# Kernel optimization log

Measured on AMD Instinct MI355X. Metric: run time of the kernel, lower is better.

Reference implementation:

```python
import jax, jax.numpy as jnp
import numpy as np

N_NODES = 100000
N_EDGES = 3200000
IN_F, HID, N_CLS = 10, 64, 10
NEG_SLOPE = 0.01  # torch default for F.leaky_relu


def gcn_conv(h, src, dst, W, b, n_nodes):
    h = h @ W  # transform first (small feature dim -> cheap)
    # self loops
    loop = jnp.arange(n_nodes, dtype=src.dtype)
    s = jnp.concatenate([src, loop])
    d = jnp.concatenate([dst, loop])
    deg = jax.ops.segment_sum(jnp.ones_like(d, dtype=h.dtype), d, num_segments=n_nodes)
    dinv = jnp.where(deg > 0, jax.lax.rsqrt(deg), 0.0)
    norm = dinv[s] * dinv[d]  # [E+N]
    msg = h[s] * norm[:, None]  # gather + scale
    out = jax.ops.segment_sum(msg, d, num_segments=n_nodes)  # scatter-add
    return out + b


def setup_inputs() -> dict:
    key = jax.random.key(0)
    ks = jax.random.split(key, 10)
    x = jax.random.normal(ks[0], (N_NODES, IN_F), dtype=jnp.float32)
    edge_index = jax.random.randint(ks[1], (2, N_EDGES), 0, N_NODES, dtype=jnp.int64)
    def glorot(k, fan_in, fan_out):
        lim = np.sqrt(6.0 / (fan_in + fan_out))
        return jax.random.uniform(k, (fan_in, fan_out), jnp.float32, -lim, lim)
    W1 = glorot(ks[2], IN_F, HID)
    b1 = jnp.zeros((HID,), jnp.float32)
    W2 = glorot(ks[3], HID, HID)
    b2 = jnp.zeros((HID,), jnp.float32)
    W3 = glorot(ks[4], HID, HID)
    b3 = jnp.zeros((HID,), jnp.float32)
    Wfc = glorot(ks[5], HID, N_CLS)
    bfc = jnp.zeros((N_CLS,), jnp.float32)
    return {"x": x, "edge_index": edge_index, "W1": W1, "b1": b1,
            "W2": W2, "b2": b2, "W3": W3, "b3": b3, "Wfc": Wfc, "bfc": bfc}


def reference(x, edge_index, W1, b1, W2, b2, W3, b3, Wfc, bfc):
    src, dst = edge_index[0], edge_index[1]
    n = x.shape[0]
    h = jax.nn.leaky_relu(gcn_conv(x, src, dst, W1, b1, n), NEG_SLOPE)
    h = jax.nn.leaky_relu(gcn_conv(h, src, dst, W2, b2, n), NEG_SLOPE)
    h = jax.nn.leaky_relu(gcn_conv(h, src, dst, W3, b3, n), NEG_SLOPE)
    return h @ Wfc + bfc
```

## Files before the change

### kernel.cpp

```cpp
#include <hip/hip_runtime.h>
#include <hip/hip_fp16.h>

#define N_NODES_C 100000
#define N_EDGES_C 3200000
#define IN_F_C 10
#define HID_C 64
#define N_CLS_C 10
#define NEG_SLOPE_C 0.01f

#define NBUCK 98
#define BCAP  36864
#define TILE  2048

typedef _Float16 f16x2 __attribute__((ext_vector_type(2)));

__device__ __forceinline__ float fdot2(unsigned int a, unsigned int b, float c) {
#if defined(__has_builtin) && __has_builtin(__builtin_amdgcn_fdot2)
    return __builtin_amdgcn_fdot2(__builtin_bit_cast(f16x2, a), __builtin_bit_cast(f16x2, b), c, false);
#else
    __half2 ah = __builtin_bit_cast(__half2, a), bh = __builtin_bit_cast(__half2, b);
    float2 af = __half22float2(ah), bf = __half22float2(bh);
    return c + af.x * bf.x + af.y * bf.y;
#endif
}

__global__ __launch_bounds__(256) void k_bucket(const int* __restrict__ src,
                                                const int* __restrict__ dst,
                                                int* __restrict__ bcur,
                                                int* __restrict__ pairs, int E) {
    __shared__ int lcnt[NBUCK];
    __shared__ int gbase[NBUCK];
    const int t = threadIdx.x;
    for (int i = t; i < NBUCK; i += 256) lcnt[i] = 0;
    __syncthreads();
    const int base = blockIdx.x * TILE;
    int p[8], r[8], nb[8];
#pragma unroll
    for (int i = 0; i < 8; ++i) {
        int e = base + t + i * 256;
        if (e < E) {
            int s = src[e], d = dst[e];
            int b = d >> 10;
            nb[i] = b;
            p[i] = (s << 10) | (d & 1023);
            r[i] = atomicAdd(&lcnt[b], 1);
        }
    }
    __syncthreads();
    for (int i = t; i < NBUCK; i += 256)
        gbase[i] = lcnt[i] ? atomicAdd(&bcur[i], lcnt[i]) : 0;
    __syncthreads();
#pragma unroll
    for (int i = 0; i < 8; ++i) {
        int e = base + t + i * 256;
        if (e < E) {
            int pos = gbase[nb[i]] + r[i];
            if (pos < BCAP) pairs[nb[i] * BCAP + pos] = p[i];
        }
    }
}

__global__ __launch_bounds__(128) void k_bscan(const int* __restrict__ bcur,
                                               int* __restrict__ bOff, int nbk) {
    __shared__ int s[128];
    int t = threadIdx.x;
    int v = (t < nbk) ? bcur[t] : 0;
    s[t] = v;
    __syncthreads();
    for (int off = 1; off < 128; off <<= 1) {
        int u = (t >= off) ? s[t - off] : 0;
        __syncthreads();
        s[t] += u;
        __syncthreads();
    }
    if (t < nbk) bOff[t] = s[t] - v;
}

__global__ __launch_bounds__(1024) void k_build(const int* __restrict__ pairs,
                                                const int* __restrict__ bcur,
                                                const int* __restrict__ bOff,
                                                int* __restrict__ row_ptr,
                                                float* __restrict__ dinv,
                                                int* __restrict__ col) {
    __shared__ int hist[1024];
    __shared__ int sm[1024];
    const int b = blockIdx.x;
    const int t = threadIdx.x;
    const int n = min(bcur[b], BCAP);
    const int base = bOff[b];
    const int* pp = pairs + b * BCAP;

    hist[t] = 0;
    __syncthreads();
    for (int i = t; i < n; i += 1024) atomicAdd(&hist[pp[i] & 1023], 1);
    __syncthreads();
    int c = hist[t];
    sm[t] = c;
    __syncthreads();
    for (int off = 1; off < 1024; off <<= 1) {
        int u = (t >= off) ? sm[t - off] : 0;
        __syncthreads();
        sm[t] += u;
        __syncthreads();
    }
    int rp = base + sm[t] - c;
    int gnode = (b << 10) + t;
    if (gnode < N_NODES_C) {
        row_ptr[gnode] = rp;
        dinv[gnode] = rsqrtf((float)(c + 1));
        if (gnode == N_NODES_C - 1) row_ptr[N_NODES_C] = rp + c;
    }
    __syncthreads();
    sm[t] = rp;
    __syncthreads();
    for (int i = t; i < n; i += 1024) {
        int p = pp[i];
        int idx = atomicAdd(&sm[p & 1023], 1);
        col[idx] = p >> 10;
    }
}

__global__ __launch_bounds__(256) void k_mm0(const float* __restrict__ x,
                                             const float* __restrict__ W,
                                             const float* __restrict__ dinv,
                                             __half* __restrict__ hs, int n) {
    __shared__ float4 W4[IN_F_C * 16];
    const int t = threadIdx.x;
    for (int i = t; i < IN_F_C * 16; i += 256) {
        int k = i >> 4, f4 = i & 15;
        W4[i] = ((const float4*)(W + k * HID_C))[f4];
    }
    __syncthreads();
    int idx = blockIdx.x * 256 + t;
    if (idx >= n * 16) return;
    int nn = idx >> 4, f4 = idx & 15;
    const float* row = x + nn * IN_F_C;
    float4 acc = make_float4(0.f, 0.f, 0.f, 0.f);
#pragma unroll
    for (int k = 0; k < IN_F_C; ++k) {
        float xv = row[k];
        float4 w = W4[k * 16 + f4];
        acc.x += xv * w.x; acc.y += xv * w.y; acc.z += xv * w.z; acc.w += xv * w.w;
    }
    float di = dinv[nn];
    ((__half2*)hs)[(nn << 5) + 2 * f4]     = __floats2half2_rn(acc.x * di, acc.y * di);
    ((__half2*)hs)[(nn << 5) + 2 * f4 + 1] = __floats2half2_rn(acc.z * di, acc.w * di);
}

__global__ __launch_bounds__(256) void k_wcvt(const float* __restrict__ W, uint4* __restrict__ wh) {
    int i = blockIdx.x * 256 + threadIdx.x;
    if (i >= 8 * HID_C) return;
    int k8 = i >> 6, f = i & 63;
    __half2 h[4];
#pragma unroll
    for (int j = 0; j < 4; ++j)
        h[j] = __floats2half2_rn(W[(8 * k8 + 2 * j) * HID_C + f],
                                 W[(8 * k8 + 2 * j + 1) * HID_C + f]);
    wh[i] = *(uint4*)h;
}

__global__ __launch_bounds__(256) void k_gftL(const int* __restrict__ row_ptr,
                                              const int* __restrict__ col,
                                              const __half2* __restrict__ hs,
                                              const float* __restrict__ dinv,
                                              const float* __restrict__ bias,
                                              const uint4* __restrict__ wh,
                                              __half* __restrict__ hnext, int n) {
    __shared__ uint4 WhL[8 * HID_C];
    __shared__ __half2 rowh[4][32];
    const int t = threadIdx.x;
#pragma unroll
    for (int i = 0; i < 2; ++i) WhL[t + i * 256] = wh[t + i * 256];
    __syncthreads();

    const int lane = t & 63;
    const int wid  = t >> 6;
    const int half = lane >> 5;
    const int fl   = lane & 31;
    const int d = (blockIdx.x << 2) + wid;
    if (d >= n) return;
    const int beg = row_ptr[d];
    const int end = row_ptr[d + 1];

    float2 acc = make_float2(0.f, 0.f);
    if (!half) {
        float2 v = __half22float2(hs[(d << 5) + fl]);
        acc.x = v.x; acc.y = v.y;
    }
    int e = beg;
    for (; e + 7 < end; e += 8) {
        int i0 = e + half, i1 = e + 2 + half, i2 = e + 4 + half, i3 = e + 6 + half;
        int s0 = col[i0], s1 = col[i1], s2 = col[i2], s3 = col[i3];
        float2 v0 = __half22float2(hs[(s0 << 5) + fl]);
        float2 v1 = __half22float2(hs[(s1 << 5) + fl]);
        float2 v2 = __half22float2(hs[(s2 << 5) + fl]);
        float2 v3 = __half22float2(hs[(s3 << 5) + fl]);
        acc.x += v0.x + v1.x + v2.x + v3.x;
        acc.y += v0.y + v1.y + v2.y + v3.y;
    }
    for (; e < end; e += 2) {
        int i = e + half;
        if (i < end) {
            float2 v = __half22float2(hs[(col[i] << 5) + fl]);
            acc.x += v.x; acc.y += v.y;
        }
    }
    acc.x += __shfl_xor(acc.x, 32, 64);
    acc.y += __shfl_xor(acc.y, 32, 64);

    const float di = dinv[d];
    if (!half) {
        float2 bb = ((const float2*)bias)[fl];
        float vx = acc.x * di + bb.x;
        float vy = acc.y * di + bb.y;
        vx = vx > 0.f ? vx : NEG_SLOPE_C * vx;
        vy = vy > 0.f ? vy : NEG_SLOPE_C * vy;
        rowh[wid][fl] = __floats2half2_rn(vx, vy);
    }
    {
        float s = 0.f;
        const uint4* rq = (const uint4*)rowh[wid];
#pragma unroll
        for (int k8 = 0; k8 < 8; ++k8) {
            uint4 wv = WhL[(k8 << 6) + lane];
            uint4 rv = rq[k8];
            s = fdot2(rv.x, wv.x, s);
            s = fdot2(rv.y, wv.y, s);
            s = fdot2(rv.z, wv.z, s);
            s = fdot2(rv.w, wv.w, s);
        }
        hnext[(d << 6) + lane] = __float2half(s * di);
    }
}

__global__ __launch_bounds__(256) void k_gfcL(const int* __restrict__ row_ptr,
                                              const int* __restrict__ col,
                                              const __half2* __restrict__ hs,
                                              const float* __restrict__ dinv,
                                              const float* __restrict__ bias,
                                              const float* __restrict__ Wn,
                                              const float* __restrict__ bn,
                                              float* __restrict__ out, int n) {
    __shared__ float4 Ws4[16 * N_CLS_C];
    __shared__ float rowbuf[4][64];
    const int t = threadIdx.x;
    for (int i = t; i < 16 * N_CLS_C; i += 256) {
        int k4 = i / N_CLS_C, f = i - k4 * N_CLS_C;
        Ws4[i] = make_float4(Wn[(4 * k4 + 0) * N_CLS_C + f], Wn[(4 * k4 + 1) * N_CLS_C + f],
                             Wn[(4 * k4 + 2) * N_CLS_C + f], Wn[(4 * k4 + 3) * N_CLS_C + f]);
    }
    __syncthreads();

    const int lane = t & 63;
    const int wid  = t >> 6;
    const int half = lane >> 5;
    const int fl   = lane & 31;
    const int d = (blockIdx.x << 2) + wid;
    if (d >= n) return;
    const int beg = row_ptr[d];
    const int end = row_ptr[d + 1];

    float2 acc = make_float2(0.f, 0.f);
    if (!half) {
        float2 v = __half22float2(hs[(d << 5) + fl]);
        acc.x = v.x; acc.y = v.y;
    }
    int e = beg;
    for (; e + 7 < end; e += 8) {
        int i0 = e + half, i1 = e + 2 + half, i2 = e + 4 + half, i3 = e + 6 + half;
        int s0 = col[i0], s1 = col[i1], s2 = col[i2], s3 = col[i3];
        float2 v0 = __half22float2(hs[(s0 << 5) + fl]);
        float2 v1 = __half22float2(hs[(s1 << 5) + fl]);
        float2 v2 = __half22float2(hs[(s2 << 5) + fl]);
        float2 v3 = __half22float2(hs[(s3 << 5) + fl]);
        acc.x += v0.x + v1.x + v2.x + v3.x;
        acc.y += v0.y + v1.y + v2.y + v3.y;
    }
    for (; e < end; e += 2) {
        int i = e + half;
        if (i < end) {
            float2 v = __half22float2(hs[(col[i] << 5) + fl]);
            acc.x += v.x; acc.y += v.y;
        }
    }
    acc.x += __shfl_xor(acc.x, 32, 64);
    acc.y += __shfl_xor(acc.y, 32, 64);

    const float di = dinv[d];
    if (!half) {
        float2 bb = ((const float2*)bias)[fl];
        float vx = acc.x * di + bb.x;
        float vy = acc.y * di + bb.y;
        vx = vx > 0.f ? vx : NEG_SLOPE_C * vx;
        vy = vy > 0.f ? vy : NEG_SLOPE_C * vy;
        ((float2*)rowbuf[wid])[fl] = make_float2(vx, vy);
    }
    if (lane < N_CLS_C) {
        float s = bn[lane];
        const float4* rb = (const float4*)rowbuf[wid];
#pragma unroll
        for (int k4 = 0; k4 < 16; ++k4) {
            float4 r4 = rb[k4];
            float4 w4 = Ws4[k4 * N_CLS_C + lane];
            s += r4.x * w4.x + r4.y * w4.y + r4.z * w4.z + r4.w * w4.w;
        }
        out[d * N_CLS_C + lane] = s;
    }
}

extern "C" void kernel_launch(void* const* d_in, const int* in_sizes, int n_in,
                              void* d_out, int out_size, void* d_ws, size_t ws_size,
                              hipStream_t stream) {
    const float* x   = (const float*)d_in[0];
    const int*   ei  = (const int*)d_in[1];
    const float* W1  = (const float*)d_in[2];
    const float* b1  = (const float*)d_in[3];
    const float* W2  = (const float*)d_in[4];
    const float* b2  = (const float*)d_in[5];
    const float* W3  = (const float*)d_in[6];
    const float* b3  = (const float*)d_in[7];
    const float* Wfc = (const float*)d_in[8];
    const float* bfc = (const float*)d_in[9];
    float* out = (float*)d_out;

    const int N = N_NODES_C;
    const int E = N_EDGES_C;
    const int* src = ei;
    const int* dst = ei + E;

    float*  dinv    = (float*)d_ws;
    int*    bcur    = (int*)(dinv + N);
    int*    bOff    = bcur + 128;
    int*    row_ptr = bOff + 128;
    uint4*  wh2     = (uint4*)(row_ptr + N + 4);
    uint4*  wh3     = wh2 + 512;
    int*    col     = (int*)(wh3 + 512);
    int*    pairs   = col + E;
    __half* hsA     = (__half*)pairs;
    __half* hsB     = (__half*)(pairs + (size_t)NBUCK * BCAP);

    int gN4 = (N + 3) / 4;
    int gM0 = (N * 16 + 255) / 256;
    int gBK = (E + TILE - 1) / TILE;

    hipMemsetAsync(bcur, 0, 128 * sizeof(int), stream);
    k_bucket<<<gBK, 256, 0, stream>>>(src, dst, bcur, pairs, E);
    k_bscan<<<1, 128, 0, stream>>>(bcur, bOff, NBUCK);
    k_build<<<NBUCK, 1024, 0, stream>>>(pairs, bcur, bOff, row_ptr, dinv, col);

    k_wcvt<<<2, 256, 0, stream>>>(W2, wh2);
    k_wcvt<<<2, 256, 0, stream>>>(W3, wh3);

    k_mm0<<<gM0, 256, 0, stream>>>(x, W1, dinv, hsA, N);

    k_gftL<<<gN4, 256, 0, stream>>>(row_ptr, col, (const __half2*)hsA, dinv, b1, wh2, hsB, N);
    k_gftL<<<gN4, 256, 0, stream>>>(row_ptr, col, (const __half2*)hsB, dinv, b2, wh3, hsA, N);
    k_gfcL<<<gN4, 256, 0, stream>>>(row_ptr, col, (const __half2*)hsA, dinv, b3, Wfc, bfc, out, N);
}
```

Before: 440.6 us.

## Split feature matrix into two half-width planes for cache-friendly gathers

Stores the 64-wide fp16 node features as two 32-feature planes. Each aggregation layer now runs as two passes: the first gathers plane 0 and writes a partial activation, the second gathers plane 1 and then applies the dense transform. The aim is to halve the working set of each random gather (3.2 MB per plane) so it stays resident in cache, and to load column indices with non-temporal hints. In exchange the edge list is read twice per layer and the number of launches grows. The small weight-prep and bucket-scan kernels are also merged into a prep kernel and into the build kernel to cut launch overhead.

New measurement: 603.5 us. 37.0% more time.

```diff
diff --git a/kernel.cpp b/kernel.cpp
--- a/kernel.cpp
+++ b/kernel.cpp
@@ -11,6 +11,7 @@
 #define NBUCK 98
 #define BCAP  36864
 #define TILE  2048
+#define PL_H2 (N_NODES_C * 16)
 
 typedef _Float16 f16x2 __attribute__((ext_vector_type(2)));
 
@@ -24,6 +25,33 @@
 #endif
 }
 
+__global__ __launch_bounds__(256) void k_prep(const float* __restrict__ W2, const float* __restrict__ W3,
+                                              const float* __restrict__ Wfc,
+                                              uint4* __restrict__ wh2, uint4* __restrict__ wh3,
+                                              float2* __restrict__ wf2, int* __restrict__ bcur) {
+    const int b = blockIdx.x, t = threadIdx.x;
+    if (b < 2) {
+        const float* W = b ? W3 : W2;
+        uint4* wh = b ? wh3 : wh2;
+        for (int i = t; i < 8 * HID_C; i += 256) {
+            int k8 = i >> 6, f = i & 63;
+            __half2 h[4];
+#pragma unroll
+            for (int j = 0; j < 4; ++j)
+                h[j] = __floats2half2_rn(W[(8 * k8 + 2 * j) * HID_C + f],
+                                         W[(8 * k8 + 2 * j + 1) * HID_C + f]);
+            wh[i] = *(uint4*)h;
+        }
+    } else if (b == 2) {
+        for (int i = t; i < 32 * N_CLS_C; i += 256) {
+            int k2 = i / N_CLS_C, c = i - k2 * N_CLS_C;
+            wf2[i] = make_float2(Wfc[(2 * k2) * N_CLS_C + c], Wfc[(2 * k2 + 1) * N_CLS_C + c]);
+        }
+    } else {
+        if (t < 128) bcur[t] = 0;
+    }
+}
+
 __global__ __launch_bounds__(256) void k_bucket(const int* __restrict__ src,
                                                 const int* __restrict__ dst,
                                                 int* __restrict__ bcur,
@@ -60,35 +88,29 @@
     }
 }
 
-__global__ __launch_bounds__(128) void k_bscan(const int* __restrict__ bcur,
-                                               int* __restrict__ bOff, int nbk) {
-    __shared__ int s[128];
-    int t = threadIdx.x;
-    int v = (t < nbk) ? bcur[t] : 0;
-    s[t] = v;
-    __syncthreads();
-    for (int off = 1; off < 128; off <<= 1) {
-        int u = (t >= off) ? s[t - off] : 0;
-        __syncthreads();
-        s[t] += u;
-        __syncthreads();
-    }
-    if (t < nbk) bOff[t] = s[t] - v;
-}
-
 __global__ __launch_bounds__(1024) void k_build(const int* __restrict__ pairs,
                                                 const int* __restrict__ bcur,
-                                                const int* __restrict__ bOff,
                                                 int* __restrict__ row_ptr,
                                                 float* __restrict__ dinv,
                                                 int* __restrict__ col) {
     __shared__ int hist[1024];
     __shared__ int sm[1024];
+    __shared__ int bs[128];
     const int b = blockIdx.x;
     const int t = threadIdx.x;
     const int n = min(bcur[b], BCAP);
-    const int base = bOff[b];
     const int* pp = pairs + b * BCAP;
+
+    if (t < 128) bs[t] = (t < NBUCK) ? bcur[t] : 0;
+    __syncthreads();
+    for (int off = 1; off < 128; off <<= 1) {
+        int u = 0;
+        if (t < 128 && t >= off) u = bs[t - off];
+        __syncthreads();
+        if (t < 128) bs[t] += u;
+        __syncthreads();
+    }
+    const int base = (b > 0) ? bs[b - 1] : 0;
 
     hist[t] = 0;
     __syncthreads();
@@ -123,7 +145,7 @@
 __global__ __launch_bounds__(256) void k_mm0(const float* __restrict__ x,
                                              const float* __restrict__ W,
                                              const float* __restrict__ dinv,
-                                             __half* __restrict__ hs, int n) {
+                                             __half2* __restrict__ hs, int n) {
     __shared__ float4 W4[IN_F_C * 16];
     const int t = threadIdx.x;
     for (int i = t; i < IN_F_C * 16; i += 256) {
@@ -143,166 +165,203 @@
         acc.x += xv * w.x; acc.y += xv * w.y; acc.z += xv * w.z; acc.w += xv * w.w;
     }
     float di = dinv[nn];
-    ((__half2*)hs)[(nn << 5) + 2 * f4]     = __floats2half2_rn(acc.x * di, acc.y * di);
-    ((__half2*)hs)[(nn << 5) + 2 * f4 + 1] = __floats2half2_rn(acc.z * di, acc.w * di);
-}
-
-__global__ __launch_bounds__(256) void k_wcvt(const float* __restrict__ W, uint4* __restrict__ wh) {
-    int i = blockIdx.x * 256 + threadIdx.x;
-    if (i >= 8 * HID_C) return;
-    int k8 = i >> 6, f = i & 63;
-    __half2 h[4];
-#pragma unroll
-    for (int j = 0; j < 4; ++j)
-        h[j] = __floats2half2_rn(W[(8 * k8 + 2 * j) * HID_C + f],
-                                 W[(8 * k8 + 2 * j + 1) * HID_C + f]);
-    wh[i] = *(uint4*)h;
-}
-
-__global__ __launch_bounds__(256) void k_gftL(const int* __restrict__ row_ptr,
-                                              const int* __restrict__ col,
-                                              const __half2* __restrict__ hs,
-                                              const float* __restrict__ dinv,
-                                              const float* __restrict__ bias,
-                                              const uint4* __restrict__ wh,
-                                              __half* __restrict__ hnext, int n) {
-    __shared__ uint4 WhL[8 * HID_C];
-    __shared__ __half2 rowh[4][32];
-    const int t = threadIdx.x;
-#pragma unroll
-    for (int i = 0; i < 2; ++i) WhL[t + i * 256] = wh[t + i * 256];
-    __syncthreads();
-
-    const int lane = t & 63;
-    const int wid  = t >> 6;
-    const int half = lane >> 5;
-    const int fl   = lane & 31;
-    const int d = (blockIdx.x << 2) + wid;
+    int pl = f4 >> 3;
+    int qin = (2 * f4) & 15;
+    __half2* base = hs + pl * PL_H2 + (nn << 4);
+    base[qin]     = __floats2half2_rn(acc.x * di, acc.y * di);
+    base[qin + 1] = __floats2half2_rn(acc.z * di, acc.w * di);
+}
+
+__global__ __launch_bounds__(512) void k_gp0(const int* __restrict__ row_ptr,
+                                             const int* __restrict__ col,
+                                             const __half2* __restrict__ hp,
+                                             const float* __restrict__ dinv,
+                                             const float* __restrict__ bias,
+                                             unsigned int* __restrict__ act0,
+                                             int n) {
+    const int t = threadIdx.x;
+    const int lane = t & 63, wid = t >> 6;
+    const int g = lane >> 4, fl = lane & 15;
+    const int d = (blockIdx.x << 3) + wid;
     if (d >= n) return;
-    const int beg = row_ptr[d];
-    const int end = row_ptr[d + 1];
-
+    const int beg = row_ptr[d], end = row_ptr[d + 1];
     float2 acc = make_float2(0.f, 0.f);
-    if (!half) {
-        float2 v = __half22float2(hs[(d << 5) + fl]);
-        acc.x = v.x; acc.y = v.y;
-    }
+    if (g == 0) acc = __half22float2(hp[(d << 4) + fl]);
     int e = beg;
-    for (; e + 7 < end; e += 8) {
-        int i0 = e + half, i1 = e + 2 + half, i2 = e + 4 + half, i3 = e + 6 + half;
-        int s0 = col[i0], s1 = col[i1], s2 = col[i2], s3 = col[i3];
-        float2 v0 = __half22float2(hs[(s0 << 5) + fl]);
-        float2 v1 = __half22float2(hs[(s1 << 5) + fl]);
-        float2 v2 = __half22float2(hs[(s2 << 5) + fl]);
-        float2 v3 = __half22float2(hs[(s3 << 5) + fl]);
-        acc.x += v0.x + v1.x + v2.x + v3.x;
-        acc.y += v0.y + v1.y + v2.y + v3.y;
-    }
-    for (; e < end; e += 2) {
-        int i = e + half;
+    for (; e + 15 < end; e += 16) {
+        int s0 = __builtin_nontemporal_load(col + e + g);
+        int s1 = __builtin_nontemporal_load(col + e + 4 + g);
+        int s2 = __builtin_nontemporal_load(col + e + 8 + g);
+        int s3 = __builtin_nontemporal_load(col + e + 12 + g);
+        float2 v0 = __half22float2(hp[(s0 << 4) + fl]);
+        float2 v1 = __half22float2(hp[(s1 << 4) + fl]);
+        float2 v2 = __half22float2(hp[(s2 << 4) + fl]);
+        float2 v3 = __half22float2(hp[(s3 << 4) + fl]);
+        acc.x += (v0.x + v1.x) + (v2.x + v3.x);
+        acc.y += (v0.y + v1.y) + (v2.y + v3.y);
+    }
+    for (; e < end; e += 4) {
+        int i = e + g;
         if (i < end) {
-            float2 v = __half22float2(hs[(col[i] << 5) + fl]);
+            int s = __builtin_nontemporal_load(col + i);
+            float2 v = __half22float2(hp[(s << 4) + fl]);
             acc.x += v.x; acc.y += v.y;
         }
     }
-    acc.x += __shfl_xor(acc.x, 32, 64);
-    acc.y += __shfl_xor(acc.y, 32, 64);
-
-    const float di = dinv[d];
-    if (!half) {
+    acc.x += __shfl_xor(acc.x, 16, 64); acc.y += __shfl_xor(acc.y, 16, 64);
+    acc.x += __shfl_xor(acc.x, 32, 64); acc.y += __shfl_xor(acc.y, 32, 64);
+    if (g == 0) {
+        float di = dinv[d];
         float2 bb = ((const float2*)bias)[fl];
         float vx = acc.x * di + bb.x;
         float vy = acc.y * di + bb.y;
         vx = vx > 0.f ? vx : NEG_SLOPE_C * vx;
         vy = vy > 0.f ? vy : NEG_SLOPE_C * vy;
-        rowh[wid][fl] = __floats2half2_rn(vx, vy);
-    }
-    {
-        float s = 0.f;
-        const uint4* rq = (const uint4*)rowh[wid];
-#pragma unroll
-        for (int k8 = 0; k8 < 8; ++k8) {
-            uint4 wv = WhL[(k8 << 6) + lane];
-            uint4 rv = rq[k8];
-            s = fdot2(rv.x, wv.x, s);
-            s = fdot2(rv.y, wv.y, s);
-            s = fdot2(rv.z, wv.z, s);
-            s = fdot2(rv.w, wv.w, s);
-        }
-        hnext[(d << 6) + lane] = __float2half(s * di);
-    }
-}
-
-__global__ __launch_bounds__(256) void k_gfcL(const int* __restrict__ row_ptr,
+        __half2 h = __floats2half2_rn(vx, vy);
+        __builtin_nontemporal_store(__builtin_bit_cast(unsigned int, h), act0 + (d << 4) + fl);
+    }
+}
+
+__global__ __launch_bounds__(512) void k_gp1T(const int* __restrict__ row_ptr,
                                               const int* __restrict__ col,
-                                              const __half2* __restrict__ hs,
+                                              const __half2* __restrict__ hp,
+                                              const unsigned int* __restrict__ act0,
                                               const float* __restrict__ dinv,
                                               const float* __restrict__ bias,
-                                              const float* __restrict__ Wn,
-                                              const float* __restrict__ bn,
-                                              float* __restrict__ out, int n) {
-    __shared__ float4 Ws4[16 * N_CLS_C];
-    __shared__ float rowbuf[4][64];
-    const int t = threadIdx.x;
-    for (int i = t; i < 16 * N_CLS_C; i += 256) {
-        int k4 = i / N_CLS_C, f = i - k4 * N_CLS_C;
-        Ws4[i] = make_float4(Wn[(4 * k4 + 0) * N_CLS_C + f], Wn[(4 * k4 + 1) * N_CLS_C + f],
-                             Wn[(4 * k4 + 2) * N_CLS_C + f], Wn[(4 * k4 + 3) * N_CLS_C + f]);
-    }
-    __syncthreads();
-
-    const int lane = t & 63;
-    const int wid  = t >> 6;
-    const int half = lane >> 5;
-    const int fl   = lane & 31;
-    const int d = (blockIdx.x << 2) + wid;
+                                              const uint4* __restrict__ wh,
+                                              __half* __restrict__ hnext,
+                                              int n) {
+    __shared__ uint4 WhL[8 * HID_C];
+    __shared__ __half2 rowh[8][32];
+    const int t = threadIdx.x;
+    WhL[t] = wh[t];
+    __syncthreads();
+
+    const int lane = t & 63, wid = t >> 6;
+    const int g = lane >> 4, fl = lane & 15;
+    const int d = (blockIdx.x << 3) + wid;
     if (d >= n) return;
-    const int beg = row_ptr[d];
-    const int end = row_ptr[d + 1];
-
+    const int beg = row_ptr[d], end = row_ptr[d + 1];
     float2 acc = make_float2(0.f, 0.f);
-    if (!half) {
-        float2 v = __half22float2(hs[(d << 5) + fl]);
-        acc.x = v.x; acc.y = v.y;
-    }
+    if (g == 0) acc = __half22float2(hp[(d << 4) + fl]);
     int e = beg;
-    for (; e + 7 < end; e += 8) {
-        int i0 = e + half, i1 = e + 2 + half, i2 = e + 4 + half, i3 = e + 6 + half;
-        int s0 = col[i0], s1 = col[i1], s2 = col[i2], s3 = col[i3];
-        float2 v0 = __half22float2(hs[(s0 << 5) + fl]);
-        float2 v1 = __half22float2(hs[(s1 << 5) + fl]);
-        float2 v2 = __half22float2(hs[(s2 << 5) + fl]);
-        float2 v3 = __half22float2(hs[(s3 << 5) + fl]);
-        acc.x += v0.x + v1.x + v2.x + v3.x;
-        acc.y += v0.y + v1.y + v2.y + v3.y;
-    }
-    for (; e < end; e += 2) {
-        int i = e + half;
+    for (; e + 15 < end; e += 16) {
+        int s0 = __builtin_nontemporal_load(col + e + g);
+        int s1 = __builtin_nontemporal_load(col + e + 4 + g);
+        int s2 = __builtin_nontemporal_load(col + e + 8 + g);
+        int s3 = __builtin_nontemporal_load(col + e + 12 + g);
+        float2 v0 = __half22float2(hp[(s0 << 4) + fl]);
+        float2 v1 = __half22float2(hp[(s1 << 4) + fl]);
+        float2 v2 = __half22float2(hp[(s2 << 4) + fl]);
+        float2 v3 = __half22float2(hp[(s3 << 4) + fl]);
+        acc.x += (v0.x + v1.x) + (v2.x + v3.x);
+        acc.y += (v0.y + v1.y) + (v2.y + v3.y);
+    }
+    for (; e < end; e += 4) {
+        int i = e + g;
         if (i < end) {
-            float2 v = __half22float2(hs[(col[i] << 5) + fl]);
+            int s = __builtin_nontemporal_load(col + i);
+            float2 v = __half22float2(hp[(s << 4) + fl]);
             acc.x += v.x; acc.y += v.y;
         }
     }
-    acc.x += __shfl_xor(acc.x, 32, 64);
-    acc.y += __shfl_xor(acc.y, 32, 64);
+    acc.x += __shfl_xor(acc.x, 16, 64); acc.y += __shfl_xor(acc.y, 16, 64);
+    acc.x += __shfl_xor(acc.x, 32, 64); acc.y += __shfl_xor(acc.y, 32, 64);
 
     const float di = dinv[d];
-    if (!half) {
-        float2 bb = ((const float2*)bias)[fl];
+    if (lane < 16)
+        rowh[wid][lane] = __builtin_bit_cast(__half2, __builtin_nontemporal_load(act0 + (d << 4) + lane));
+    if (g == 0) {
+        float2 bb = ((const float2*)bias)[16 + fl];
         float vx = acc.x * di + bb.x;
         float vy = acc.y * di + bb.y;
         vx = vx > 0.f ? vx : NEG_SLOPE_C * vx;
         vy = vy > 0.f ? vy : NEG_SLOPE_C * vy;
-        ((float2*)rowbuf[wid])[fl] = make_float2(vx, vy);
+        rowh[wid][16 + fl] = __floats2half2_rn(vx, vy);
+    }
+    float s = 0.f;
+    const uint4* rq = (const uint4*)rowh[wid];
+#pragma unroll
+    for (int k8 = 0; k8 < 8; ++k8) {
+        uint4 wv = WhL[(k8 << 6) + lane];
+        uint4 rv = rq[k8];
+        s = fdot2(rv.x, wv.x, s);
+        s = fdot2(rv.y, wv.y, s);
+        s = fdot2(rv.z, wv.z, s);
+        s = fdot2(rv.w, wv.w, s);
+    }
+    int pl = lane >> 5, fi = lane & 31;
+    hnext[(size_t)pl * (N_NODES_C * 32) + d * 32 + fi] = __float2half(s * di);
+}
+
+__global__ __launch_bounds__(512) void k_gpF(const int* __restrict__ row_ptr,
+                                             const int* __restrict__ col,
+                                             const __half2* __restrict__ hp,
+                                             const unsigned int* __restrict__ act0,
+                                             const float* __restrict__ dinv,
+                                             const float* __restrict__ bias,
+                                             const float2* __restrict__ wf2,
+                                             const float* __restrict__ bn,
+                                             float* __restrict__ out, int n) {
+    __shared__ float2 Wf2[32 * N_CLS_C];
+    __shared__ float bL[N_CLS_C];
+    __shared__ float2 rowf[8][32];
+    const int t = threadIdx.x;
+    if (t < 32 * N_CLS_C) Wf2[t] = wf2[t];
+    if (t < N_CLS_C) bL[t] = bn[t];
+    __syncthreads();
+
+    const int lane = t & 63, wid = t >> 6;
+    const int g = lane >> 4, fl = lane & 15;
+    const int d = (blockIdx.x << 3) + wid;
+    if (d >= n) return;
+    const int beg = row_ptr[d], end = row_ptr[d + 1];
+    float2 acc = make_float2(0.f, 0.f);
+    if (g == 0) acc = __half22float2(hp[(d << 4) + fl]);
+    int e = beg;
+    for (; e + 15 < end; e += 16) {
+        int s0 = __builtin_nontemporal_load(col + e + g);
+        int s1 = __builtin_nontemporal_load(col + e + 4 + g);
+        int s2 = __builtin_nontemporal_load(col + e + 8 + g);
+        int s3 = __builtin_nontemporal_load(col + e + 12 + g);
+        float2 v0 = __half22float2(hp[(s0 << 4) + fl]);
+        float2 v1 = __half22float2(hp[(s1 << 4) + fl]);
+        float2 v2 = __half22float2(hp[(s2 << 4) + fl]);
+        float2 v3 = __half22float2(hp[(s3 << 4) + fl]);
+        acc.x += (v0.x + v1.x) + (v2.x + v3.x);
+        acc.y += (v0.y + v1.y) + (v2.y + v3.y);
+    }
+    for (; e < end; e += 4) {
+        int i = e + g;
+        if (i < end) {
+            int s = __builtin_nontemporal_load(col + i);
+            float2 v = __half22float2(hp[(s << 4) + fl]);
+            acc.x += v.x; acc.y += v.y;
+        }
+    }
+    acc.x += __shfl_xor(acc.x, 16, 64); acc.y += __shfl_xor(acc.y, 16, 64);
+    acc.x += __shfl_xor(acc.x, 32, 64); acc.y += __shfl_xor(acc.y, 32, 64);
+
+    const float di = dinv[d];
+    if (lane < 16) {
+        __half2 h = __builtin_bit_cast(__half2, __builtin_nontemporal_load(act0 + (d << 4) + lane));
+        rowf[wid][lane] = __half22float2(h);
+    }
+    if (g == 0) {
+        float2 bb = ((const float2*)bias)[16 + fl];
+        float vx = acc.x * di + bb.x;
+        float vy = acc.y * di + bb.y;
+        vx = vx > 0.f ? vx : NEG_SLOPE_C * vx;
+        vy = vy > 0.f ? vy : NEG_SLOPE_C * vy;
+        rowf[wid][16 + fl] = make_float2(vx, vy);
     }
     if (lane < N_CLS_C) {
-        float s = bn[lane];
-        const float4* rb = (const float4*)rowbuf[wid];
-#pragma unroll
-        for (int k4 = 0; k4 < 16; ++k4) {
-            float4 r4 = rb[k4];
-            float4 w4 = Ws4[k4 * N_CLS_C + lane];
-            s += r4.x * w4.x + r4.y * w4.y + r4.z * w4.z + r4.w * w4.w;
+        float s = bL[lane];
+#pragma unroll
+        for (int k2 = 0; k2 < 32; ++k2) {
+            float2 a = rowf[wid][k2];
+            float2 w = Wf2[k2 * N_CLS_C + lane];
+            s += a.x * w.x + a.y * w.y;
         }
         out[d * N_CLS_C + lane] = s;
     }
@@ -330,30 +389,36 @@
 
     float*  dinv    = (float*)d_ws;
     int*    bcur    = (int*)(dinv + N);
-    int*    bOff    = bcur + 128;
-    int*    row_ptr = bOff + 128;
+    int*    row_ptr = bcur + 128;
     uint4*  wh2     = (uint4*)(row_ptr + N + 4);
     uint4*  wh3     = wh2 + 512;
-    int*    col     = (int*)(wh3 + 512);
+    float2* wf2     = (float2*)(wh3 + 512);
+    int*    col     = (int*)(wf2 + 320);
     int*    pairs   = col + E;
     __half* hsA     = (__half*)pairs;
     __half* hsB     = (__half*)(pairs + (size_t)NBUCK * BCAP);
-
-    int gN4 = (N + 3) / 4;
+    unsigned int* act0 = (unsigned int*)(hsB + (size_t)N * HID_C);
+
+    int gN8 = (N + 7) / 8;
     int gM0 = (N * 16 + 255) / 256;
     int gBK = (E + TILE - 1) / TILE;
 
-    hipMemsetAsync(bcur, 0, 128 * sizeof(int), stream);
+    __half2* hsA0 = (__half2*)hsA;
+    __half2* hsA1 = hsA0 + PL_H2;
+    __half2* hsB0 = (__half2*)hsB;
+    __half2* hsB1 = hsB0 + PL_H2;
+
+    k_prep<<<4, 256, 0, stream>>>(W2, W3, Wfc, wh2, wh3, wf2, bcur);
+
     k_bucket<<<gBK, 256, 0, stream>>>(src, dst, bcur, pairs, E);
-    k_bscan<<<1, 128, 0, stream>>>(bcur, bOff, NBUCK);
-    k_build<<<NBUCK, 1024, 0, stream>>>(pairs, bcur, bOff, row_ptr, dinv, col);
-
-    k_wcvt<<<2, 256, 0, stream>>>(W2, wh2);
-    k_wcvt<<<2, 256, 0, stream>>>(W3, wh3);
-
-    k_mm0<<<gM0, 256, 0, stream>>>(x, W1, dinv, hsA, N);
-
-    k_gftL<<<gN4, 256, 0, stream>>>(row_ptr, col, (const __half2*)hsA, dinv, b1, wh2, hsB, N);
-    k_gftL<<<gN4, 256, 0, stream>>>(row_ptr, col, (const __half2*)hsB, dinv, b2, wh3, hsA, N);
-    k_gfcL<<<gN4, 256, 0, stream>>>(row_ptr, col, (const __half2*)hsA, dinv, b3, Wfc, bfc, out, N);
-}
+    k_build<<<NBUCK, 1024, 0, stream>>>(pairs, bcur, row_ptr, dinv, col);
+
+    k_mm0<<<gM0, 256, 0, stream>>>(x, W1, dinv, (__half2*)hsA, N);
+
+    k_gp0 <<<gN8, 512, 0, stream>>>(row_ptr, col, hsA0, dinv, b1, act0, N);
+    k_gp1T<<<gN8, 512, 0, stream>>>(row_ptr, col, hsA1, act0, dinv, b1, wh2, hsB, N);
+    k_gp0 <<<gN8, 512, 0, stream>>>(row_ptr, col, hsB0, dinv, b2, act0, N);
+    k_gp1T<<<gN8, 512, 0, stream>>>(row_ptr, col, hsB1, act0, dinv, b2, wh3, hsA, N);
+    k_gp0 <<<gN8, 512, 0, stream>>>(row_ptr, col, hsA0, dinv, b3, act0, N);
+    k_gpF <<<gN8, 512, 0, stream>>>(row_ptr, col, hsA1, act0, dinv, b3, wf2, bfc, out, N);
+}
```
